# Optimization experiments

Hardware: AMD Instinct MI355X
Metric: run time of the kernel (lower is better)

The kernel has to match this reference:

```python
import jax, jax.numpy as jnp
import numpy as np

# dims
B, T = 2, 256
E = 512            # n_embd
G = 8              # n_groups
GD = E // G        # group_dim == head_dim == 64
L = 8              # n_layer
N = L * G          # n_nodes == 64
V = 50257          # vocab
S = 8              # n_steps


def _rms(x):
    eps = jnp.asarray(jnp.finfo(x.dtype).eps, x.dtype)
    return x * jax.lax.rsqrt(jnp.mean(x * x, axis=-1, keepdims=True) + eps)


def _rope(x, cos, sin):
    # x: (B,T,N,GD); cos/sin: (T, GD//2)
    d = x.shape[-1] // 2
    x1, x2 = x[..., :d], x[..., d:]
    c = cos[None, :, None, :]
    s = sin[None, :, None, :]
    return jnp.concatenate([x1 * c + x2 * s, -x1 * s + x2 * c], axis=-1)


def setup_inputs() -> dict:
    key = jax.random.key(0)
    ks = jax.random.split(key, 9)
    idx = jax.random.randint(ks[0], (B, T), 0, V, dtype=jnp.int32)
    wte = 0.02 * jax.random.normal(ks[1], (V, E), jnp.float32)
    # adapters: identity block at group slice (per init_weights) + small noise
    ad = np.zeros((N, GD, E), np.float32)
    for i in range(N):
        g = i % G
        ad[i, :, g * GD:(g + 1) * GD] = np.eye(GD, dtype=np.float32)
    adapters = jnp.asarray(ad) + 0.005 * jax.random.normal(ks[2], (N, GD, E), jnp.float32)
    qkv_w = 0.005 * jax.random.normal(ks[3], (N, 3 * GD, GD), jnp.float32)
    attn_proj = 0.005 * jax.random.normal(ks[4], (N, GD, GD), jnp.float32)
    mlp_fc = 0.005 * jax.random.normal(ks[5], (N, 4 * GD, GD), jnp.float32)
    mlp_proj = 0.005 * jax.random.normal(ks[6], (N, GD, 4 * GD), jnp.float32)
    # structured dependency matrix: layer l <- layer l-1, weight 1/G
    D = np.zeros((N, N), np.float32)
    for l in range(1, L):
        D[l * G:(l + 1) * G, (l - 1) * G:l * G] = 1.0 / G
    dep = jnp.asarray(D)
    router_w = (1.0 / np.sqrt(E)) * jax.random.normal(ks[7], (E, 1), jnp.float32)
    router_b = jnp.full((1,), -3.0, jnp.float32)
    lm_head_w = 0.005 * jax.random.normal(ks[8], (V, E), jnp.float32)
    return {"idx": idx, "n_steps": S, "wte": wte, "adapters": adapters,
            "qkv_w": qkv_w, "attn_proj": attn_proj, "mlp_fc": mlp_fc,
            "mlp_proj": mlp_proj, "dep": dep, "router_w": router_w,
            "router_b": router_b, "lm_head_w": lm_head_w}


def _forward(idx, n_steps, wte, adapters, qkv_w, attn_proj, mlp_fc, mlp_proj,
             dep, router_w, router_b, lm_head_w):
    Bs, Ts = idx.shape
    groups = np.arange(N) % G  # static scatter/gather pattern: node -> group slice
    inv_freq = 1.0 / (10000.0 ** (np.arange(0, GD, 2, dtype=np.float64) / GD))
    freqs = np.outer(np.arange(Ts), inv_freq)
    cos = jnp.asarray(np.cos(freqs), jnp.float32)
    sin = jnp.asarray(np.sin(freqs), jnp.float32)

    x = _rms(wte[idx])                                  # (B,T,E)
    p_cont = jnp.ones((Bs, Ts), x.dtype)

    # depths computed under no_grad in torch -> stop_gradient here
    dp = jax.nn.relu(jax.lax.stop_gradient(dep))
    depths = jnp.zeros((N,), x.dtype)
    for _ in range(L):
        depths = dp @ (depths + 1.0)

    causal = np.tril(np.ones((Ts, Ts), bool))
    scale = 1.0 / np.sqrt(GD)

    for t in range(n_steps):
        td = t * (L / n_steps)
        w_all = jnp.exp(-jnp.abs(depths - td))
        # torch gathers active = w_all > 0.15; equivalent dense form: zero-weight inactive
        w_eff = jnp.where(w_all > 0.15, w_all, jnp.zeros_like(w_all))

        xi = (jnp.einsum('bte,nge->btng', x, adapters)
              + x.reshape(Bs, Ts, G, GD)[:, :, groups, :])          # (B,T,N,GD)
        qkv = jnp.einsum('btng,nog->btno', xi, qkv_w).reshape(Bs, Ts, N, 3, GD)
        q, k, v = qkv[..., 0, :], qkv[..., 1, :], qkv[..., 2, :]
        q = _rms(_rope(q, cos, sin))
        k = _rms(_rope(k, cos, sin))
        scores = jnp.einsum('btng,bsng->bnts', q, k) * scale
        scores = jnp.where(causal[None, None], scores, -jnp.inf)
        att = jnp.einsum('bnts,bsng->btng', jax.nn.softmax(scores, axis=-1), v)
        # NOTE: einsum strings below intentionally replicate the original code
        # (k and o are summed out without contraction against the other operand)
        xi_mid = xi + jnp.einsum('btng,ngk->btng', att, attn_proj)
        fc = jnp.einsum('btng,nog->btno', _rms(xi_mid), mlp_fc)
        mp = jnp.einsum('btno,ngk->btng', jnp.square(jax.nn.relu(fc)), mlp_proj)
        up = (xi_mid + mp - xi) * w_eff[None, None, :, None]
        # scatter-add back by group (node n = l*G + g -> group g)
        full_up = up.reshape(Bs, Ts, L, G, GD).sum(axis=2).reshape(Bs, Ts, E)
        x = x + full_up * p_cont[..., None]
        # router (training-mode soft halting; top_fixed=bottom_fixed=0)
        ph = jax.nn.sigmoid(x @ router_w + router_b)[..., 0]
        p_cont = p_cont * (1.0 - ph)

    logits = _rms(x) @ lm_head_w.T
    return 15.0 * jnp.tanh(logits / 15.0)


def reference(idx, n_steps, wte, adapters, qkv_w, attn_proj, mlp_fc, mlp_proj,
              dep, router_w, router_b, lm_head_w):
    return _forward(idx, n_steps, wte, adapters, qkv_w, attn_proj, mlp_fc,
                    mlp_proj, dep, router_w, router_b, lm_head_w)
```

## Files before the change

kernel.cpp:

```cpp
#include <hip/hip_runtime.h>
#include <hip/hip_bf16.h>
#include <math.h>

#define BB 2
#define TT 256
#define BT 512
#define EE 512
#define GG 8
#define GD 64
#define LL 8
#define NN 64
#define VV 50257
#define D2 32
#define EPS 1.1920928955078125e-07f
#define S72 72

typedef __attribute__((ext_vector_type(4))) float floatx4;
typedef __attribute__((ext_vector_type(8))) short short8;

struct __attribute__((packed, aligned(4))) f4u { float x, y, z, w; };

#define OFF_DEPTHS   0
#define OFF_APS      64
#define OFF_MPS      (OFF_APS + NN*GD)
#define OFF_COS      (OFF_MPS + NN*GD)
#define OFF_SIN      (OFF_COS + TT*D2)
#define OFF_X        (OFF_SIN + TT*D2)
#define OFF_PCONT    (OFF_X + BT*EE)
#define OFF_SMLP     (OFF_PCONT + BT)
#define OFF_YBF      (OFF_SMLP + BT*NN)
#define OFF_STEP     (OFF_YBF + (BT*EE)/2)
#define OFF_XI       OFF_STEP
#define OFF_ATT      (OFF_XI + BT*NN*GD)
#define OFF_XBF      (OFF_ATT + BT*NN*GD)
#define OFF_QB       (OFF_XBF + (BT*EE)/2)
#define OFF_KB       (OFF_QB + (BT*NN*GD)/2)
#define OFF_VTB      (OFF_KB + (BT*NN*GD)/2)
#define OFF_ABF      (OFF_VTB + (BT*NN*GD)/2)
#define OFF_QWBF     (OFF_ABF + (NN*GD*EE)/2)
#define OFF_FWBF     (OFF_QWBF + (NN*192*GD)/2)
#define OFF_WBF      OFF_STEP

__device__ __forceinline__ float step_weight(const float* depths, const int* ns, int t, int n) {
    float td = (float)t * (8.0f / (float)ns[0]);
    float wa = expf(-fabsf(depths[n] - td));
    return (wa > 0.15f) ? wa : 0.0f;
}

__device__ __forceinline__ float fast_tanh15(float v) {
    float u = v * (1.f/15.f);
    float e = __expf(2.f * u);
    return 15.f * (1.f - __fdividef(2.f, e + 1.f));
}

__global__ void k_prep(const float* __restrict__ dep, float* __restrict__ depths) {
    __shared__ float cur[NN], nxt[NN];
    int i = threadIdx.x;
    if (i < NN) cur[i] = 0.f;
    __syncthreads();
    for (int it = 0; it < LL; ++it) {
        if (i < NN) {
            float acc = 0.f;
            for (int m = 0; m < NN; ++m) acc += fmaxf(dep[i*NN + m], 0.f) * (cur[m] + 1.f);
            nxt[i] = acc;
        }
        __syncthreads();
        if (i < NN) cur[i] = nxt[i];
        __syncthreads();
    }
    if (i < NN) depths[i] = cur[i];
}

__global__ void k_sums(const float* __restrict__ attn_proj, const float* __restrict__ mlp_proj,
                       float* __restrict__ aps, float* __restrict__ mps) {
    int i = blockIdx.x * blockDim.x + threadIdx.x;
    if (i >= NN*GD) return;
    float a = 0.f;
    const float* ap = attn_proj + (size_t)i * GD;
    for (int k = 0; k < GD; ++k) a += ap[k];
    aps[i] = a;
    float m = 0.f;
    const float* mp = mlp_proj + (size_t)i * 4 * GD;
    for (int k = 0; k < 4*GD; ++k) m += mp[k];
    mps[i] = m;
}

__global__ void k_rope_table(float* __restrict__ ctab, float* __restrict__ stab) {
    int i = blockIdx.x * blockDim.x + threadIdx.x;
    if (i >= TT*D2) return;
    int pos = i / D2, f = i % D2;
    double inv = pow(10000.0, -((double)(2*f)) / (double)GD);
    double ang = (double)pos * inv;
    ctab[i] = (float)cos(ang);
    stab[i] = (float)sin(ang);
}

__global__ void k_cvt(const float* __restrict__ src, __hip_bfloat16* __restrict__ dst, int n4) {
    int i = blockIdx.x * blockDim.x + threadIdx.x;
    if (i >= n4) return;
    float4 f = ((const float4*)src)[i];
    __hip_bfloat16 h0 = __float2bfloat16(f.x);
    __hip_bfloat16 h1 = __float2bfloat16(f.y);
    __hip_bfloat16 h2 = __float2bfloat16(f.z);
    __hip_bfloat16 h3 = __float2bfloat16(f.w);
    ushort4 o;
    o.x = *(const unsigned short*)&h0;
    o.y = *(const unsigned short*)&h1;
    o.z = *(const unsigned short*)&h2;
    o.w = *(const unsigned short*)&h3;
    *(ushort4*)(dst + (size_t)i*4) = o;
}

__global__ void k_embed(const int* __restrict__ idx, const float* __restrict__ wte,
                        float* __restrict__ x, __hip_bfloat16* __restrict__ xbf,
                        float* __restrict__ pcont) {
    int bt = blockIdx.x;
    int tid = threadIdx.x;
    const float* src = wte + (size_t)idx[bt] * EE;
    float v0 = src[tid], v1 = src[tid + 256];
    __shared__ float red[4];
    float ss = v0*v0 + v1*v1;
    for (int o = 32; o > 0; o >>= 1) ss += __shfl_xor(ss, o);
    if ((tid & 63) == 0) red[tid >> 6] = ss;
    __syncthreads();
    float sc = rsqrtf((red[0]+red[1]+red[2]+red[3]) / (float)EE + EPS);
    float a = v0 * sc, b = v1 * sc;
    x[bt*EE + tid]       = a;
    x[bt*EE + tid + 256] = b;
    xbf[bt*EE + tid]       = __float2bfloat16(a);
    xbf[bt*EE + tid + 256] = __float2bfloat16(b);
    if (tid == 0) pcont[bt] = 1.f;
}

__global__ __launch_bounds__(256) void k_xi_qkv(const __hip_bfloat16* __restrict__ xbf,
        const __hip_bfloat16* __restrict__ abf, const __hip_bfloat16* __restrict__ qwbf,
        const float* __restrict__ x, float* __restrict__ xi,
        __hip_bfloat16* __restrict__ qb, __hip_bfloat16* __restrict__ kb,
        __hip_bfloat16* __restrict__ vtb,
        const float* __restrict__ ctab, const float* __restrict__ stab,
        const float* __restrict__ depths, const int* __restrict__ ns, int t) {
    int n = blockIdx.y;
    if (step_weight(depths, ns, t, n) == 0.f) return;
    int bt0 = blockIdx.x * 64;
    __shared__ __align__(16) char smem[16640 + 16384 + 9216];
    __hip_bfloat16* sA   = (__hip_bfloat16*)smem;
    float*          obuf = (float*)smem;
    __hip_bfloat16* sB   = (__hip_bfloat16*)(smem + 16640);
    __hip_bfloat16* Bs72 = (__hip_bfloat16*)(smem + 16640);
    __hip_bfloat16* xis  = (__hip_bfloat16*)(smem + 33024);
    int tid = threadIdx.x;
    int wave = tid >> 6, lane = tid & 63;
    int wr = wave >> 1, wc = wave & 1;
    int quad = lane >> 4, l16 = lane & 15;

    size_t goffA[2], goffB[2];
    int sOff[2];
    #pragma unroll
    for (int j = 0; j < 2; ++j) {
        int s = (j*4 + wave)*64 + lane;
        int r = s >> 3;
        int cs = (s & 7) ^ (r & 7);
        goffA[j] = (size_t)(bt0 + r)*EE + cs*8;
        goffB[j] = ((size_t)n*GD + r)*EE + cs*8;
        sOff[j] = (j*4 + wave)*512;
    }

    floatx4 acc[2][2];
    #pragma unroll
    for (int mt = 0; mt < 2; ++mt)
        #pragma unroll
        for (int nt = 0; nt < 2; ++nt) acc[mt][nt] = (floatx4){0.f,0.f,0.f,0.f};

    #pragma unroll
    for (int j = 0; j < 2; ++j) {
        __builtin_amdgcn_global_load_lds(
            (const __attribute__((address_space(1))) void*)(xbf + goffA[j]),
            (__attribute__((address_space(3))) void*)(&sA[sOff[j]]), 16, 0, 0);
        __builtin_amdgcn_global_load_lds(
            (const __attribute__((address_space(1))) void*)(abf + goffB[j]),
            (__attribute__((address_space(3))) void*)(&sB[sOff[j]]), 16, 0, 0);
    }
    __syncthreads();

    int cur = 0;
    #pragma unroll
    for (int kt = 0; kt < 8; ++kt) {
        if (kt < 7) {
            int k0 = (kt + 1) * 64;
            #pragma unroll
            for (int j = 0; j < 2; ++j) {
                __builtin_amdgcn_global_load_lds(
                    (const __attribute__((address_space(1))) void*)(xbf + goffA[j] + k0),
                    (__attribute__((address_space(3))) void*)(&sA[(cur^1)*4096 + sOff[j]]), 16, 0, 0);
                __builtin_amdgcn_global_load_lds(
                    (const __attribute__((address_space(1))) void*)(abf + goffB[j] + k0),
                    (__attribute__((address_space(3))) void*)(&sB[(cur^1)*4096 + sOff[j]]), 16, 0, 0);
            }
        }
        #pragma unroll
        for (int ks = 0; ks < 2; ++ks) {
            short8 af[2], bf[2];
            #pragma unroll
            for (int mt = 0; mt < 2; ++mt) {
                int row = wr*32 + mt*16 + l16;
                int ck = ((ks << 2) | quad) ^ (row & 7);
                af[mt] = *(const short8*)(&sA[cur*4096 + row*64 + ck*8]);
            }
            #pragma unroll
            for (int nt = 0; nt < 2; ++nt) {
                int row = wc*32 + nt*16 + l16;
                int ck = ((ks << 2) | quad) ^ (row & 7);
                bf[nt] = *(const short8*)(&sB[cur*4096 + row*64 + ck*8]);
            }
            #pragma unroll
            for (int mt = 0; mt < 2; ++mt)
                #pragma unroll
                for (int nt = 0; nt < 2; ++nt)
                    acc[mt][nt] = __builtin_amdgcn_mfma_f32_16x16x32_bf16(af[mt], bf[nt], acc[mt][nt], 0, 0, 0);
        }
        __syncthreads();
        cur ^= 1;
    }

    int gofs = (n & (GG-1)) * GD;
    #pragma unroll
    for (int mt = 0; mt < 2; ++mt) {
        #pragma unroll
        for (int nt = 0; nt < 2; ++nt) {
            int col = wc*32 + nt*16 + l16;
            #pragma unroll
            for (int r = 0; r < 4; ++r) {
                int token = wr*32 + mt*16 + quad*4 + r;
                int bt = bt0 + token;
                float val = acc[mt][nt][r] + x[(size_t)bt*EE + gofs + col];
                xi[((size_t)bt*NN + n)*GD + col] = val;
                xis[token*S72 + col] = __float2bfloat16(val);
            }
        }
    }
    __syncthreads();

    const __hip_bfloat16* wbase = qwbf + (size_t)n * 192 * GD;
    int b = bt0 >> 8;
    int t0 = bt0 & (TT - 1);
    for (int c = 0; c < 3; ++c) {
        for (int i = tid; i < 512; i += 256) {
            int r = i >> 3, c8 = (i & 7) * 8;
            *(uint4*)(&Bs72[r*S72 + c8]) = *(const uint4*)(&wbase[(size_t)(c*64 + r)*GD + c8]);
        }
        __syncthreads();
        floatx4 oacc[2][2];
        #pragma unroll
        for (int mt = 0; mt < 2; ++mt)
            #pragma unroll
            for (int nt = 0; nt < 2; ++nt) oacc[mt][nt] = (floatx4){0.f,0.f,0.f,0.f};
        #pragma unroll
        for (int ks = 0; ks < 2; ++ks) {
            short8 af[2], bf[2];
            #pragma unroll
            for (int mt = 0; mt < 2; ++mt)
                af[mt] = *(const short8*)(&xis[(wr*32 + mt*16 + l16)*S72 + ks*32 + quad*8]);
            #pragma unroll
            for (int nt = 0; nt < 2; ++nt)
                bf[nt] = *(const short8*)(&Bs72[(wc*32 + nt*16 + l16)*S72 + ks*32 + quad*8]);
            #pragma unroll
            for (int mt = 0; mt < 2; ++mt)
                #pragma unroll
                for (int nt = 0; nt < 2; ++nt)
                    oacc[mt][nt] = __builtin_amdgcn_mfma_f32_16x16x32_bf16(af[mt], bf[nt], oacc[mt][nt], 0, 0, 0);
        }
        #pragma unroll
        for (int mt = 0; mt < 2; ++mt)
            #pragma unroll
            for (int nt = 0; nt < 2; ++nt)
                #pragma unroll
                for (int r = 0; r < 4; ++r)
                    obuf[(wr*32 + mt*16 + quad*4 + r)*65 + wc*32 + nt*16 + l16] = oacc[mt][nt][r];
        __syncthreads();
        if (c < 2) {
            __hip_bfloat16* dst = (c == 0) ? qb : kb;
            for (int tr = 0; tr < 16; ++tr) {
                int row = wave*16 + tr, bt = bt0 + row;
                float val = obuf[row*65 + lane];
                int pos = bt & (TT - 1);
                float pair = __shfl_xor(val, 32);
                int fi = lane & 31;
                float cc = ctab[pos*D2 + fi], sn = stab[pos*D2 + fi];
                float nv = (lane < 32) ? (val*cc + pair*sn) : (val*cc - pair*sn);
                float ss = nv*nv;
                for (int o = 32; o > 0; o >>= 1) ss += __shfl_xor(ss, o);
                float outv = nv * rsqrtf(ss / (float)GD + EPS);
                dst[((size_t)bt*NN + n)*GD + lane] = __float2bfloat16(outv);
            }
        } else {
            for (int tr = 0; tr < 16; ++tr) {
                int g = wave*16 + tr;
                float vv = obuf[lane*65 + g];
                vtb[(((size_t)(b*NN + n))*GD + g)*TT + t0 + lane] = __float2bfloat16(vv);
            }
        }
        __syncthreads();
    }
}

__global__ __launch_bounds__(256) void k_attn(const __hip_bfloat16* __restrict__ qb,
        const __hip_bfloat16* __restrict__ kb, const __hip_bfloat16* __restrict__ vtb,
        float* __restrict__ att,
        const float* __restrict__ depths, const int* __restrict__ ns, int t) {
    int it = blockIdx.x, b = blockIdx.y, n = blockIdx.z;
    if (step_weight(depths, ns, t, n) == 0.f) return;
    __shared__ __align__(16) __hip_bfloat16 qs[64*S72];
    __shared__ __align__(16) __hip_bfloat16 ksm[64*S72];
    __shared__ __align__(16) __hip_bfloat16 vs[64*S72];
    __shared__ __align__(16) __hip_bfloat16 ps[64*S72];
    int tid = threadIdx.x;
    int wave = tid >> 6, lane = tid & 63;
    int quad = lane >> 4, l16 = lane & 15;
    for (int i = tid; i < 512; i += 256) {
        int r = i >> 3, c8 = (i & 7) * 8;
        *(uint4*)(&qs[r*S72 + c8]) = *(const uint4*)(&qb[(((size_t)(b*TT + it*64 + r))*NN + n)*GD + c8]);
    }
    floatx4 oacc[4];
    float m_i[4], l_i[4];
    #pragma unroll
    for (int nt = 0; nt < 4; ++nt) oacc[nt] = (floatx4){0.f,0.f,0.f,0.f};
    #pragma unroll
    for (int r = 0; r < 4; ++r) { m_i[r] = -INFINITY; l_i[r] = 0.f; }
    __syncthreads();
    for (int ct = 0; ct <= it; ++ct) {
        for (int i = tid; i < 512; i += 256) {
            int r = i >> 3, c8 = (i & 7) * 8;
            *(uint4*)(&ksm[r*S72 + c8]) = *(const uint4*)(&kb[(((size_t)(b*TT + ct*64 + r))*NN + n)*GD + c8]);
            *(uint4*)(&vs[r*S72 + c8])  = *(const uint4*)(&vtb[(((size_t)(b*NN + n))*GD + r)*TT + ct*64 + c8]);
        }
        __syncthreads();
        floatx4 s[4];
        #pragma unroll
        for (int nt = 0; nt < 4; ++nt) s[nt] = (floatx4){0.f,0.f,0.f,0.f};
        #pragma unroll
        for (int ks = 0; ks < 2; ++ks) {
            short8 af = *(const short8*)(&qs[(wave*16 + l16)*S72 + ks*32 + quad*8]);
            #pragma unroll
            for (int nt = 0; nt < 4; ++nt) {
                short8 bf = *(const short8*)(&ksm[(nt*16 + l16)*S72 + ks*32 + quad*8]);
                s[nt] = __builtin_amdgcn_mfma_f32_16x16x32_bf16(af, bf, s[nt], 0, 0, 0);
            }
        }
        #pragma unroll
        for (int r = 0; r < 4; ++r) {
            int rowg = it*64 + wave*16 + quad*4 + r;
            float mx = -INFINITY;
            #pragma unroll
            for (int nt = 0; nt < 4; ++nt) {
                int colg = ct*64 + nt*16 + l16;
                float sv = (colg <= rowg) ? s[nt][r] * 0.125f : -INFINITY;
                s[nt][r] = sv;
                mx = fmaxf(mx, sv);
            }
            for (int o = 8; o > 0; o >>= 1) mx = fmaxf(mx, __shfl_xor(mx, o));
            float mnew = fmaxf(m_i[r], mx);
            float alpha = expf(m_i[r] - mnew);
            float rs = 0.f;
            #pragma unroll
            for (int nt = 0; nt < 4; ++nt) {
                float p = expf(s[nt][r] - mnew);
                s[nt][r] = p;
                rs += p;
            }
            for (int o = 8; o > 0; o >>= 1) rs += __shfl_xor(rs, o);
            l_i[r] = l_i[r]*alpha + rs;
            m_i[r] = mnew;
            #pragma unroll
            for (int nt = 0; nt < 4; ++nt) oacc[nt][r] *= alpha;
        }
        #pragma unroll
        for (int nt = 0; nt < 4; ++nt)
            #pragma unroll
            for (int r = 0; r < 4; ++r)
                ps[(wave*16 + quad*4 + r)*S72 + nt*16 + l16] = __float2bfloat16(s[nt][r]);
        __syncthreads();
        #pragma unroll
        for (int ks = 0; ks < 2; ++ks) {
            short8 af = *(const short8*)(&ps[(wave*16 + l16)*S72 + ks*32 + quad*8]);
            #pragma unroll
            for (int nt = 0; nt < 4; ++nt) {
                short8 bf = *(const short8*)(&vs[(nt*16 + l16)*S72 + ks*32 + quad*8]);
                oacc[nt] = __builtin_amdgcn_mfma_f32_16x16x32_bf16(af, bf, oacc[nt], 0, 0, 0);
            }
        }
        __syncthreads();
    }
    #pragma unroll
    for (int r = 0; r < 4; ++r) {
        float inv = 1.f / l_i[r];
        int token = it*64 + wave*16 + quad*4 + r;
        #pragma unroll
        for (int nt = 0; nt < 4; ++nt)
            att[((size_t)(b*TT + token)*NN + n)*GD + nt*16 + l16] = oacc[nt][r] * inv;
    }
}

__global__ __launch_bounds__(256) void k_fc2(const float* __restrict__ xi, const float* __restrict__ att,
        const float* __restrict__ aps, const __hip_bfloat16* __restrict__ fwbf, float* __restrict__ smlp,
        const float* __restrict__ depths, const int* __restrict__ ns, int t) {
    int n = blockIdx.y;
    if (step_weight(depths, ns, t, n) == 0.f) return;
    int bt0 = blockIdx.x * 64;
    __shared__ __align__(16) __hip_bfloat16 ys[64*S72];
    __shared__ __align__(16) __hip_bfloat16 ws[64*S72];
    __shared__ float sred[64];
    int tid = threadIdx.x;
    int wave = tid >> 6, lane = tid & 63;
    int quad = lane >> 4, l16 = lane & 15;
    for (int tr = 0; tr < 16; ++tr) {
        int row = wave*16 + tr, bt = bt0 + row;
        size_t base = ((size_t)bt*NN + n)*GD + lane;
        float xv = xi[base] + att[base] * aps[n*GD + lane];
        float ss = xv*xv;
        for (int o = 32; o > 0; o >>= 1) ss += __shfl_xor(ss, o);
        ys[row*S72 + lane] = __float2bfloat16(xv * rsqrtf(ss / (float)GD + EPS));
    }
    __syncthreads();
    float rowacc[4] = {0.f, 0.f, 0.f, 0.f};
    for (int c = 0; c < 4; ++c) {
        for (int i = tid; i < 512; i += 256) {
            int r = i >> 3, c8 = (i & 7) * 8;
            *(uint4*)(&ws[r*S72 + c8]) = *(const uint4*)(&fwbf[((size_t)n*256 + c*64 + r)*GD + c8]);
        }
        __syncthreads();
        floatx4 s[4];
        #pragma unroll
        for (int nt = 0; nt < 4; ++nt) s[nt] = (floatx4){0.f,0.f,0.f,0.f};
        #pragma unroll
        for (int ks = 0; ks < 2; ++ks) {
            short8 af = *(const short8*)(&ys[(wave*16 + l16)*S72 + ks*32 + quad*8]);
            #pragma unroll
            for (int nt = 0; nt < 4; ++nt) {
                short8 bf = *(const short8*)(&ws[(nt*16 + l16)*S72 + ks*32 + quad*8]);
                s[nt] = __builtin_amdgcn_mfma_f32_16x16x32_bf16(af, bf, s[nt], 0, 0, 0);
            }
        }
        #pragma unroll
        for (int nt = 0; nt < 4; ++nt)
            #pragma unroll
            for (int r = 0; r < 4; ++r) {
                float rr = fmaxf(s[nt][r], 0.f);
                rowacc[r] += rr*rr;
            }
        __syncthreads();
    }
    #pragma unroll
    for (int r = 0; r < 4; ++r) {
        for (int o = 8; o > 0; o >>= 1) rowacc[r] += __shfl_xor(rowacc[r], o);
        if (l16 == 0) sred[wave*16 + quad*4 + r] = rowacc[r];
    }
    __syncthreads();
    if (tid < 64) smlp[(size_t)(bt0 + tid)*NN + n] = sred[tid];
}

__global__ __launch_bounds__(256) void k_update(float* __restrict__ x, __hip_bfloat16* __restrict__ xbf,
                                                float* __restrict__ pcont,
                                                const float* __restrict__ att, const float* __restrict__ smlp,
                                                const float* __restrict__ aps, const float* __restrict__ mps,
                                                const float* __restrict__ router_w, const float* __restrict__ router_b,
                                                const float* __restrict__ depths, const int* __restrict__ ns, int t,
                                                int last, __hip_bfloat16* __restrict__ ybf) {
    int bt = blockIdx.x, tid = threadIdx.x;
    __shared__ float we[NN];
    __shared__ float red[4];
    __shared__ float red2[4];
    if (tid < NN) we[tid] = step_weight(depths, ns, t, tid);
    __syncthreads();
    float pc = pcont[bt];
    float dot = 0.f, ssq = 0.f;
    float xv0 = 0.f, xv1 = 0.f;
    #pragma unroll
    for (int h = 0; h < 2; ++h) {
        int e = tid + h*256;
        int gq = e >> 6, gd = e & 63;
        float sum = 0.f;
        #pragma unroll
        for (int l = 0; l < LL; ++l) {
            int n = l*GG + gq;
            float w = we[n];
            if (w != 0.f) {
                sum += (att[((size_t)bt*NN + n)*GD + gd] * aps[n*GD + gd]
                        + smlp[bt*NN + n] * mps[n*GD + gd]) * w;
            }
        }
        float xv = x[bt*EE + e] + sum * pc;
        x[bt*EE + e] = xv;
        if (!last) xbf[bt*EE + e] = __float2bfloat16(xv);
        dot += xv * router_w[e];
        ssq += xv * xv;
        if (h == 0) xv0 = xv; else xv1 = xv;
    }
    for (int o = 32; o > 0; o >>= 1) dot += __shfl_xor(dot, o);
    if (last) for (int o = 32; o > 0; o >>= 1) ssq += __shfl_xor(ssq, o);
    if ((tid & 63) == 0) { red[tid >> 6] = dot; red2[tid >> 6] = ssq; }
    __syncthreads();
    if (last) {
        float sc = rsqrtf((red2[0]+red2[1]+red2[2]+red2[3]) / (float)EE + EPS);
        ybf[bt*EE + tid]       = __float2bfloat16(xv0 * sc);
        ybf[bt*EE + tid + 256] = __float2bfloat16(xv1 * sc);
    }
    if (tid == 0) {
        float z = red[0]+red[1]+red[2]+red[3] + router_b[0];
        float ph = 1.f / (1.f + expf(-z));
        pcont[bt] = pc * (1.f - ph);
    }
}

__global__ __launch_bounds__(256) void k_lmhead(const __hip_bfloat16* __restrict__ ybf,
                                                const __hip_bfloat16* __restrict__ wbf,
                                                float* __restrict__ out) {
    int id = blockIdx.x;
    int w = (id & 7) * 200 + (id >> 3);
    int bm = w & 3;
    int bn = w >> 2;
    if (bn >= (VV + 127)/128) return;

    __shared__ __align__(16) char smem[32768];
    __hip_bfloat16* As  = (__hip_bfloat16*)smem;
    __hip_bfloat16* Bs  = (__hip_bfloat16*)(smem + 16384);
    float*          ebuf = (float*)smem;

    int tid = threadIdx.x;
    int wave = tid >> 6, lane = tid & 63;
    int wr = wave >> 1, wc = wave & 1;
    int quad = lane >> 4, l16 = lane & 15;

    size_t offA[4], offB[4];
    int ldsOff[4];
    #pragma unroll
    for (int j = 0; j < 4; ++j) {
        int s = (j*4 + wave)*64 + lane;
        int r = s >> 3;
        int cs = (s & 7) ^ (r & 7);
        offA[j] = (size_t)(bm*128 + r)*EE + cs*8;
        int vrow = bn*128 + r; if (vrow >= VV) vrow = VV - 1;
        offB[j] = (size_t)vrow*EE + cs*8;
        ldsOff[j] = (j*4 + wave)*512;
    }

    floatx4 acc[4][4];
    #pragma unroll
    for (int mt = 0; mt < 4; ++mt)
        #pragma unroll
        for (int nt = 0; nt < 4; ++nt)
            acc[mt][nt] = (floatx4){0.f, 0.f, 0.f, 0.f};

    for (int k0 = 0; k0 < EE; k0 += 64) {
        #pragma unroll
        for (int j = 0; j < 4; ++j) {
            __builtin_amdgcn_global_load_lds(
                (const __attribute__((address_space(1))) void*)(ybf + offA[j] + k0),
                (__attribute__((address_space(3))) void*)(&As[ldsOff[j]]), 16, 0, 0);
            __builtin_amdgcn_global_load_lds(
                (const __attribute__((address_space(1))) void*)(wbf + offB[j] + k0),
                (__attribute__((address_space(3))) void*)(&Bs[ldsOff[j]]), 16, 0, 0);
        }
        __syncthreads();
        #pragma unroll
        for (int ks = 0; ks < 2; ++ks) {
            short8 af[4], bf[4];
            #pragma unroll
            for (int mt = 0; mt < 4; ++mt) {
                int r = wr*64 + mt*16 + l16;
                int ck = ((ks << 2) | quad) ^ (r & 7);
                af[mt] = *(const short8*)(&As[r*64 + ck*8]);
            }
            #pragma unroll
            for (int nt = 0; nt < 4; ++nt) {
                int r = wc*64 + nt*16 + l16;
                int ck = ((ks << 2) | quad) ^ (r & 7);
                bf[nt] = *(const short8*)(&Bs[r*64 + ck*8]);
            }
            #pragma unroll
            for (int mt = 0; mt < 4; ++mt)
                #pragma unroll
                for (int nt = 0; nt < 4; ++nt)
                    acc[mt][nt] = __builtin_amdgcn_mfma_f32_16x16x32_bf16(af[mt], bf[nt], acc[mt][nt], 0, 0, 0);
        }
        __syncthreads();
    }

    bool lastbn = (bn == (VV >> 7));
    #pragma unroll
    for (int mt = 0; mt < 4; ++mt) {
        #pragma unroll
        for (int nt = 0; nt < 4; ++nt)
            #pragma unroll
            for (int r = 0; r < 4; ++r)
                ebuf[(wr*16 + quad*4 + r)*132 + wc*64 + nt*16 + l16] = acc[mt][nt][r];
        __syncthreads();
        #pragma unroll
        for (int p = 0; p < 4; ++p) {
            int idx = p*256 + tid;
            int row = idx >> 5;
            int col = (idx & 31) * 4;
            float4 v = *(const float4*)(&ebuf[row*132 + col]);
            float o0 = fast_tanh15(v.x);
            float o1 = fast_tanh15(v.y);
            float o2 = fast_tanh15(v.z);
            float o3 = fast_tanh15(v.w);
            int grow = bm*128 + (row >> 4)*64 + mt*16 + (row & 15);
            int gcol = bn*128 + col;
            if (!lastbn) {
                f4u s; s.x = o0; s.y = o1; s.z = o2; s.w = o3;
                *(f4u*)(&out[(size_t)grow*VV + gcol]) = s;
            } else {
                if (gcol + 0 < VV) out[(size_t)grow*VV + gcol + 0] = o0;
                if (gcol + 1 < VV) out[(size_t)grow*VV + gcol + 1] = o1;
                if (gcol + 2 < VV) out[(size_t)grow*VV + gcol + 2] = o2;
                if (gcol + 3 < VV) out[(size_t)grow*VV + gcol + 3] = o3;
            }
        }
        __syncthreads();
    }
}

extern "C" void kernel_launch(void* const* d_in, const int* in_sizes, int n_in,
                              void* d_out, int out_size, void* d_ws, size_t ws_size,
                              hipStream_t stream) {
    (void)in_sizes; (void)n_in; (void)out_size; (void)ws_size;
    const int*   idx       = (const int*)d_in[0];
    const int*   nsteps    = (const int*)d_in[1];
    const float* wte       = (const float*)d_in[2];
    const float* adapters  = (const float*)d_in[3];
    const float* qkv_w     = (const float*)d_in[4];
    const float* attn_proj = (const float*)d_in[5];
    const float* mlp_fc    = (const float*)d_in[6];
    const float* mlp_proj  = (const float*)d_in[7];
    const float* dep       = (const float*)d_in[8];
    const float* router_w  = (const float*)d_in[9];
    const float* router_b  = (const float*)d_in[10];
    const float* lm_head   = (const float*)d_in[11];
    float* out = (float*)d_out;
    float* ws  = (float*)d_ws;

    float* depths = ws + OFF_DEPTHS;
    float* aps    = ws + OFF_APS;
    float* mps    = ws + OFF_MPS;
    float* ctab   = ws + OFF_COS;
    float* stab   = ws + OFF_SIN;
    float* x      = ws + OFF_X;
    float* pcont  = ws + OFF_PCONT;
    float* smlp   = ws + OFF_SMLP;
    float* xi     = ws + OFF_XI;
    float* att    = ws + OFF_ATT;
    __hip_bfloat16* xbf  = (__hip_bfloat16*)(ws + OFF_XBF);
    __hip_bfloat16* qb   = (__hip_bfloat16*)(ws + OFF_QB);
    __hip_bfloat16* kb   = (__hip_bfloat16*)(ws + OFF_KB);
    __hip_bfloat16* vtb  = (__hip_bfloat16*)(ws + OFF_VTB);
    __hip_bfloat16* abf  = (__hip_bfloat16*)(ws + OFF_ABF);
    __hip_bfloat16* qwbf = (__hip_bfloat16*)(ws + OFF_QWBF);
    __hip_bfloat16* fwbf = (__hip_bfloat16*)(ws + OFF_FWBF);
    __hip_bfloat16* wbf  = (__hip_bfloat16*)(ws + OFF_WBF);
    __hip_bfloat16* ybf  = (__hip_bfloat16*)(ws + OFF_YBF);

    k_prep<<<1, 64, 0, stream>>>(dep, depths);
    k_sums<<<(NN*GD + 255)/256, 256, 0, stream>>>(attn_proj, mlp_proj, aps, mps);
    k_rope_table<<<(TT*D2 + 255)/256, 256, 0, stream>>>(ctab, stab);
    k_cvt<<<(NN*GD*EE/4 + 255)/256, 256, 0, stream>>>(adapters, abf, NN*GD*EE/4);
    k_cvt<<<(NN*192*GD/4 + 255)/256, 256, 0, stream>>>(qkv_w, qwbf, NN*192*GD/4);
    k_cvt<<<(NN*256*GD/4 + 255)/256, 256, 0, stream>>>(mlp_fc, fwbf, NN*256*GD/4);
    k_embed<<<BT, 256, 0, stream>>>(idx, wte, x, xbf, pcont);

    for (int t = 0; t < 8; ++t) {
        k_xi_qkv<<<dim3(BT/64, NN), 256, 0, stream>>>(xbf, abf, qwbf, x, xi, qb, kb, vtb,
                                                      ctab, stab, depths, nsteps, t);
        k_attn<<<dim3(4, BB, NN), 256, 0, stream>>>(qb, kb, vtb, att, depths, nsteps, t);
        k_fc2<<<dim3(BT/64, NN), 256, 0, stream>>>(xi, att, aps, fwbf, smlp, depths, nsteps, t);
        k_update<<<BT, 256, 0, stream>>>(x, xbf, pcont, att, smlp, aps, mps,
                                         router_w, router_b, depths, nsteps, t,
                                         (t == 7) ? 1 : 0, ybf);
    }

    k_cvt<<<((VV*EE)/4 + 255)/256, 256, 0, stream>>>(lm_head, wbf, (VV*EE)/4);
    k_lmhead<<<1600, 256, 0, stream>>>(ybf, wbf, out);
}
```

Baseline: 714.4 us.

## Double-buffer K/V and MLP weight tiles via async global-to-LDS loads with XOR swizzle

Result: faster. 695.6 us (-2.6%).

```diff
diff --git a/kernel.cpp b/kernel.cpp
--- a/kernel.cpp
+++ b/kernel.cpp
@@ -310,12 +310,34 @@
     int it = blockIdx.x, b = blockIdx.y, n = blockIdx.z;
     if (step_weight(depths, ns, t, n) == 0.f) return;
     __shared__ __align__(16) __hip_bfloat16 qs[64*S72];
-    __shared__ __align__(16) __hip_bfloat16 ksm[64*S72];
-    __shared__ __align__(16) __hip_bfloat16 vs[64*S72];
+    __shared__ __align__(16) __hip_bfloat16 ksm[2][4096];
+    __shared__ __align__(16) __hip_bfloat16 vs[2][4096];
     __shared__ __align__(16) __hip_bfloat16 ps[64*S72];
     int tid = threadIdx.x;
     int wave = tid >> 6, lane = tid & 63;
     int quad = lane >> 4, l16 = lane & 15;
+
+    size_t koff[2], voff[2];
+    int sOff[2];
+    #pragma unroll
+    for (int j = 0; j < 2; ++j) {
+        int s = (j*4 + wave)*64 + lane;
+        int r = s >> 3;
+        int cs = (s & 7) ^ (r & 7);
+        koff[j] = (((size_t)(b*TT + r))*NN + n)*GD + cs*8;
+        voff[j] = (((size_t)(b*NN + n))*GD + r)*TT + cs*8;
+        sOff[j] = (j*4 + wave)*512;
+    }
+
+    #pragma unroll
+    for (int j = 0; j < 2; ++j) {
+        __builtin_amdgcn_global_load_lds(
+            (const __attribute__((address_space(1))) void*)(kb + koff[j]),
+            (__attribute__((address_space(3))) void*)(&ksm[0][sOff[j]]), 16, 0, 0);
+        __builtin_amdgcn_global_load_lds(
+            (const __attribute__((address_space(1))) void*)(vtb + voff[j]),
+            (__attribute__((address_space(3))) void*)(&vs[0][sOff[j]]), 16, 0, 0);
+    }
     for (int i = tid; i < 512; i += 256) {
         int r = i >> 3, c8 = (i & 7) * 8;
         *(uint4*)(&qs[r*S72 + c8]) = *(const uint4*)(&qb[(((size_t)(b*TT + it*64 + r))*NN + n)*GD + c8]);
@@ -327,13 +349,22 @@
     #pragma unroll
     for (int r = 0; r < 4; ++r) { m_i[r] = -INFINITY; l_i[r] = 0.f; }
     __syncthreads();
+
+    int cur = 0;
     for (int ct = 0; ct <= it; ++ct) {
-        for (int i = tid; i < 512; i += 256) {
-            int r = i >> 3, c8 = (i & 7) * 8;
-            *(uint4*)(&ksm[r*S72 + c8]) = *(const uint4*)(&kb[(((size_t)(b*TT + ct*64 + r))*NN + n)*GD + c8]);
-            *(uint4*)(&vs[r*S72 + c8])  = *(const uint4*)(&vtb[(((size_t)(b*NN + n))*GD + r)*TT + ct*64 + c8]);
-        }
-        __syncthreads();
+        if (ct < it) {
+            size_t kadd = (size_t)(ct + 1) * 64 * NN * GD;
+            size_t vadd = (size_t)(ct + 1) * 64;
+            #pragma unroll
+            for (int j = 0; j < 2; ++j) {
+                __builtin_amdgcn_global_load_lds(
+                    (const __attribute__((address_space(1))) void*)(kb + koff[j] + kadd),
+                    (__attribute__((address_space(3))) void*)(&ksm[cur^1][sOff[j]]), 16, 0, 0);
+                __builtin_amdgcn_global_load_lds(
+                    (const __attribute__((address_space(1))) void*)(vtb + voff[j] + vadd),
+                    (__attribute__((address_space(3))) void*)(&vs[cur^1][sOff[j]]), 16, 0, 0);
+            }
+        }
         floatx4 s[4];
         #pragma unroll
         for (int nt = 0; nt < 4; ++nt) s[nt] = (floatx4){0.f,0.f,0.f,0.f};
@@ -342,7 +373,9 @@
             short8 af = *(const short8*)(&qs[(wave*16 + l16)*S72 + ks*32 + quad*8]);
             #pragma unroll
             for (int nt = 0; nt < 4; ++nt) {
-                short8 bf = *(const short8*)(&ksm[(nt*16 + l16)*S72 + ks*32 + quad*8]);
+                int row = nt*16 + l16;
+                int ck = ((ks << 2) | quad) ^ (row & 7);
+                short8 bf = *(const short8*)(&ksm[cur][row*64 + ck*8]);
                 s[nt] = __builtin_amdgcn_mfma_f32_16x16x32_bf16(af, bf, s[nt], 0, 0, 0);
             }
         }
@@ -384,11 +417,14 @@
             short8 af = *(const short8*)(&ps[(wave*16 + l16)*S72 + ks*32 + quad*8]);
             #pragma unroll
             for (int nt = 0; nt < 4; ++nt) {
-                short8 bf = *(const short8*)(&vs[(nt*16 + l16)*S72 + ks*32 + quad*8]);
+                int row = nt*16 + l16;
+                int ck = ((ks << 2) | quad) ^ (row & 7);
+                short8 bf = *(const short8*)(&vs[cur][row*64 + ck*8]);
                 oacc[nt] = __builtin_amdgcn_mfma_f32_16x16x32_bf16(af, bf, oacc[nt], 0, 0, 0);
             }
         }
         __syncthreads();
+        cur ^= 1;
     }
     #pragma unroll
     for (int r = 0; r < 4; ++r) {
@@ -407,11 +443,29 @@
     if (step_weight(depths, ns, t, n) == 0.f) return;
     int bt0 = blockIdx.x * 64;
     __shared__ __align__(16) __hip_bfloat16 ys[64*S72];
-    __shared__ __align__(16) __hip_bfloat16 ws[64*S72];
+    __shared__ __align__(16) __hip_bfloat16 ws[2][4096];
     __shared__ float sred[64];
     int tid = threadIdx.x;
     int wave = tid >> 6, lane = tid & 63;
     int quad = lane >> 4, l16 = lane & 15;
+
+    const __hip_bfloat16* wtile = fwbf + (size_t)n * 256 * GD;
+    size_t woff[2];
+    int sOff[2];
+    #pragma unroll
+    for (int j = 0; j < 2; ++j) {
+        int s = (j*4 + wave)*64 + lane;
+        int r = s >> 3;
+        int cs = (s & 7) ^ (r & 7);
+        woff[j] = (size_t)r*GD + cs*8;
+        sOff[j] = (j*4 + wave)*512;
+    }
+    #pragma unroll
+    for (int j = 0; j < 2; ++j)
+        __builtin_amdgcn_global_load_lds(
+            (const __attribute__((address_space(1))) void*)(wtile + woff[j]),
+            (__attribute__((address_space(3))) void*)(&ws[0][sOff[j]]), 16, 0, 0);
+
     for (int tr = 0; tr < 16; ++tr) {
         int row = wave*16 + tr, bt = bt0 + row;
         size_t base = ((size_t)bt*NN + n)*GD + lane;
@@ -421,13 +475,18 @@
         ys[row*S72 + lane] = __float2bfloat16(xv * rsqrtf(ss / (float)GD + EPS));
     }
     __syncthreads();
+
     float rowacc[4] = {0.f, 0.f, 0.f, 0.f};
+    int cur = 0;
+    #pragma unroll
     for (int c = 0; c < 4; ++c) {
-        for (int i = tid; i < 512; i += 256) {
-            int r = i >> 3, c8 = (i & 7) * 8;
-            *(uint4*)(&ws[r*S72 + c8]) = *(const uint4*)(&fwbf[((size_t)n*256 + c*64 + r)*GD + c8]);
-        }
-        __syncthreads();
+        if (c < 3) {
+            #pragma unroll
+            for (int j = 0; j < 2; ++j)
+                __builtin_amdgcn_global_load_lds(
+                    (const __attribute__((address_space(1))) void*)(wtile + (c + 1)*4096 + woff[j]),
+                    (__attribute__((address_space(3))) void*)(&ws[cur^1][sOff[j]]), 16, 0, 0);
+        }
         floatx4 s[4];
         #pragma unroll
         for (int nt = 0; nt < 4; ++nt) s[nt] = (floatx4){0.f,0.f,0.f,0.f};
@@ -436,7 +495,9 @@
             short8 af = *(const short8*)(&ys[(wave*16 + l16)*S72 + ks*32 + quad*8]);
             #pragma unroll
             for (int nt = 0; nt < 4; ++nt) {
-                short8 bf = *(const short8*)(&ws[(nt*16 + l16)*S72 + ks*32 + quad*8]);
+                int row = nt*16 + l16;
+                int ck = ((ks << 2) | quad) ^ (row & 7);
+                short8 bf = *(const short8*)(&ws[cur][row*64 + ck*8]);
                 s[nt] = __builtin_amdgcn_mfma_f32_16x16x32_bf16(af, bf, s[nt], 0, 0, 0);
             }
         }
@@ -448,6 +509,7 @@
                 rowacc[r] += rr*rr;
             }
         __syncthreads();
+        cur ^= 1;
     }
     #pragma unroll
     for (int r = 0; r < 4; ++r) {
```
